# Performance work log

Hardware: AMD Instinct MI355X
Metric: run time of the kernel (lower is better)

The kernel has to match this reference:

```python
import jax, jax.numpy as jnp
import numpy as np

B, S, R, H = 64, 256, 196, 1024

def setup_inputs() -> dict:
    key = jax.random.key(0)
    ks = jax.random.split(key, 12)
    s = 0.02
    return {
        "dns_feature": jax.random.normal(ks[0], (B, S, H), jnp.float32),
        "img_features": jax.random.normal(ks[1], (B, R, H), jnp.float32),
        "W_dns1": jax.random.normal(ks[2], (H, H), jnp.float32) * s,
        "b_dns1": jax.random.normal(ks[3], (H,), jnp.float32) * s,
        "W_img1": jax.random.normal(ks[4], (H, H), jnp.float32) * s,
        "w_att1": jax.random.normal(ks[5], (2 * H,), jnp.float32) * s,
        "b_att1": jax.random.normal(ks[6], (), jnp.float32) * s,
        "W_dns2": jax.random.normal(ks[7], (H, H), jnp.float32) * s,
        "W_img2": jax.random.normal(ks[8], (H, H), jnp.float32) * s,
        "b_img2": jax.random.normal(ks[9], (H,), jnp.float32) * s,
        "w_att2": jax.random.normal(ks[10], (2 * H,), jnp.float32) * s,
        "b_att2": jax.random.normal(ks[11], (), jnp.float32) * s,
    }

def reference(dns_feature, img_features, W_dns1, b_dns1, W_img1, w_att1, b_att1,
              W_dns2, W_img2, b_img2, w_att2, b_att2):
    h = W_dns1.shape[0]
    # --- stage 1: textual attention (img queries over dns positions) ---
    # tanh(concat([img_proj, dns_proj])) then 2H->1 linear decomposes into
    # per-side dot products + broadcast add (repeat is position-wise redundant).
    dns_p1 = jnp.tanh(jnp.einsum('bsh,oh->bso', dns_feature, W_dns1) + b_dns1)  # (B,S,H)
    img_p1 = jnp.tanh(jnp.einsum('brh,oh->bro', img_features, W_img1))          # (B,R,H)
    s_img = img_p1 @ w_att1[:h]   # (B,R)  concat order: [img, dns]
    s_dns = dns_p1 @ w_att1[h:]   # (B,S)
    scores1 = s_img[:, :, None] + s_dns[:, None, :] + b_att1                    # (B,R,S)
    a1 = jax.nn.softmax(scores1, axis=-1)
    att_dns = jnp.einsum('brs,bsh->brh', a1, dns_feature)                       # (B,R,H)
    # --- stage 2: visual attention (attended-dns queries over img regions) ---
    dns_p2 = jnp.tanh(jnp.einsum('brh,oh->bro', att_dns, W_dns2))               # (B,R,H)
    img_p2 = jnp.tanh(jnp.einsum('brh,oh->bro', img_features, W_img2) + b_img2) # (B,R,H)
    t_dns = dns_p2 @ w_att2[:h]   # (B,R)  concat order: [dns, img]
    t_img = img_p2 @ w_att2[h:]   # (B,R)
    scores2 = t_dns[:, :, None] + t_img[:, None, :] + b_att2                    # (B,R,R)
    a2 = jax.nn.softmax(scores2, axis=-1)
    att_img = jnp.einsum('bij,bjh->bih', a2, img_features)                      # (B,R,H)
    return att_img, att_dns
```

## Files before the change

kernel.cpp:

```cpp
#include <hip/hip_runtime.h>

#define Hdim 1024
#define BB 64
#define SS 256
#define RR 196
#define MD (BB * SS)
#define MI (BB * RR)

typedef __attribute__((ext_vector_type(8))) short short8;
typedef __attribute__((ext_vector_type(4))) float floatx4;
typedef unsigned short us;

__device__ __forceinline__ unsigned short f2bf(float f) {
  unsigned int u = __float_as_uint(f);
  unsigned int r = 0x7FFFu + ((u >> 16) & 1u);
  return (unsigned short)((u + r) >> 16);
}

__device__ __forceinline__ float fast_tanh(float x) {
  x = fminf(15.f, fmaxf(-15.f, x));
  float e = __expf(2.f * x);
  return (e - 1.f) / (e + 1.f);
}

#define GLOAD16(g, l) __builtin_amdgcn_global_load_lds( \
    (const __attribute__((address_space(1))) unsigned int*)(g), \
    (__attribute__((address_space(3))) unsigned int*)(l), 16, 0, 0)

#define MEMFENCE asm volatile("" ::: "memory")

__global__ __launch_bounds__(256) void prep_kernel(
    const float4* __restrict__ dns, const float4* __restrict__ img,
    const float4* __restrict__ Wd1, const float4* __restrict__ Wi2,
    uint4* __restrict__ dns_bf, uint4* __restrict__ img_bf,
    uint4* __restrict__ wd1_bf, uint4* __restrict__ wi2_bf,
    float4* __restrict__ scz)
{
  constexpr int N0 = (MD * Hdim) / 8;
  constexpr int N1 = N0 + (MI * Hdim) / 8;
  constexpr int N2 = N1 + (Hdim * Hdim) / 8;
  constexpr int N3 = N2 + (Hdim * Hdim) / 8;
  constexpr int N4 = N3 + (MD + MI) / 8;
  const int stride = gridDim.x * 256;
  for (int i = blockIdx.x * 256 + threadIdx.x; i < N4; i += stride) {
    if (i < N3) {
      const float4* src; uint4* dst; int li;
      if (i < N0)      { src = dns; dst = dns_bf; li = i; }
      else if (i < N1) { src = img; dst = img_bf; li = i - N0; }
      else if (i < N2) { src = Wd1; dst = wd1_bf; li = i - N1; }
      else             { src = Wi2; dst = wi2_bf; li = i - N2; }
      const float4 a = src[2 * li];
      const float4 b = src[2 * li + 1];
      uint4 o;
      o.x = (unsigned)f2bf(a.x) | ((unsigned)f2bf(a.y) << 16);
      o.y = (unsigned)f2bf(a.z) | ((unsigned)f2bf(a.w) << 16);
      o.z = (unsigned)f2bf(b.x) | ((unsigned)f2bf(b.y) << 16);
      o.w = (unsigned)f2bf(b.z) | ((unsigned)f2bf(b.w) << 16);
      dst[li] = o;
    } else {
      const int li = i - N3;
      const float4 z4 = {0.f, 0.f, 0.f, 0.f};
      scz[2 * li]     = z4;
      scz[2 * li + 1] = z4;
    }
  }
}

#define NB1 ((MD / 256) * 4)
#define NB2 ((MI / 256) * 4)

__global__ __launch_bounds__(512, 2) void gemm_score_8p(
    const us* __restrict__ X1, const us* __restrict__ W1,
    const float* __restrict__ bias1, const float* __restrict__ v1, float* sc1,
    const us* __restrict__ X2, const us* __restrict__ W2,
    const float* __restrict__ bias2, const float* __restrict__ v2, float* sc2)
{
  __shared__ us LDS[65536];

  const int nwg = gridDim.x;
  const int q = nwg >> 3, rr = nwg & 7;
  const int xcd = blockIdx.x & 7, idx = blockIdx.x >> 3;
  const int wg = (xcd < rr ? xcd * (q + 1) : rr * (q + 1) + (xcd - rr) * q) + idx;

  const us* Xb; const us* Wb; const float* bias; const float* vatt; float* scores;
  int mt, nt;
  if (wg < NB1) {
    Xb = X1; Wb = W1; bias = bias1; vatt = v1; scores = sc1;
    mt = wg >> 2; nt = wg & 3;
  } else {
    const int w2 = wg - NB1;
    Xb = X2; Wb = W2; bias = bias2; vatt = v2; scores = sc2;
    mt = w2 >> 2; nt = w2 & 3;
  }
  const long m0 = (long)mt * 256;
  const long n0 = (long)nt * 256;

  const int tid  = threadIdx.x;
  const int lane = tid & 63;
  const int w    = tid >> 6;
  const int wm   = w >> 2;
  const int wn   = w & 3;

  const int srow = lane >> 3;
  const int scol = ((lane & 7) ^ srow) * 8;
  const us* gA = Xb + (m0 + w * 8 + srow) * Hdim + scol;
  const us* gB = Wb + (n0 + w * 8 + srow) * Hdim + scol;
  const int ldl = (w * 64 + lane) * 8;

#define STAGE_A(d, h, kk) do { \
    GLOAD16(gA + ((h) * 128 + 0) * Hdim + (kk),  &LDS[(d) * 16384 + (h) * 8192 + 0    + ldl]); \
    GLOAD16(gA + ((h) * 128 + 64) * Hdim + (kk), &LDS[(d) * 16384 + (h) * 8192 + 4096 + ldl]); } while (0)
#define STAGE_B(d, h, kk) do { \
    GLOAD16(gB + ((h) * 128 + 0) * Hdim + (kk),  &LDS[32768 + (d) * 16384 + (h) * 8192 + 0    + ldl]); \
    GLOAD16(gB + ((h) * 128 + 64) * Hdim + (kk), &LDS[32768 + (d) * 16384 + (h) * 8192 + 4096 + ldl]); } while (0)

  floatx4 acc[8][4];
  #pragma unroll
  for (int i = 0; i < 8; ++i)
    #pragma unroll
    for (int j = 0; j < 4; ++j)
      acc[i][j] = (floatx4){0.f, 0.f, 0.f, 0.f};

  const int frow = lane & 15;
  const int g    = lane >> 4;
  const int sw   = frow & 7;
  const int aRow = wm * 8192 + frow * 64;
  const int bRow = (wn >> 1) * 8192 + ((wn & 1) * 64 + frow) * 64;

  STAGE_A(0, 0, 0); STAGE_A(0, 1, 0); STAGE_B(0, 0, 0); STAGE_B(0, 1, 0);
  asm volatile("s_waitcnt vmcnt(0)" ::: "memory");
  MEMFENCE; __builtin_amdgcn_s_barrier(); MEMFENCE;

  #pragma unroll 1
  for (int T = 0; T < 16; ++T) {
    const int d   = T & 1;
    const int kk1 = (T + 1) * 64;
    const int Ab  = d * 16384 + aRow;
    const int Bb  = 32768 + d * 16384 + bRow;
    const int s0  = (g ^ sw) * 8;
    const int s1  = ((4 + g) ^ sw) * 8;
    short8 a[4], b0[4], b1[4];

    if (T < 15) { STAGE_A(d ^ 1, 0, kk1); STAGE_A(d ^ 1, 1, kk1); }
    #pragma unroll
    for (int mf = 0; mf < 4; ++mf) a[mf] = *(const short8*)&LDS[Ab + mf * 1024 + s0];
    #pragma unroll
    for (int nf = 0; nf < 4; ++nf) b0[nf] = *(const short8*)&LDS[Bb + nf * 1024 + s0];
    __builtin_amdgcn_s_setprio(1);
    #pragma unroll
    for (int mf = 0; mf < 4; ++mf)
      #pragma unroll
      for (int nf = 0; nf < 4; ++nf)
        acc[mf][nf] = __builtin_amdgcn_mfma_f32_16x16x32_bf16(a[mf], b0[nf], acc[mf][nf], 0, 0, 0);
    __builtin_amdgcn_s_setprio(0);
    MEMFENCE; __builtin_amdgcn_s_barrier(); MEMFENCE;

    if (T < 15) { STAGE_B(d ^ 1, 0, kk1); STAGE_B(d ^ 1, 1, kk1); }
    #pragma unroll
    for (int mf = 0; mf < 4; ++mf) a[mf] = *(const short8*)&LDS[Ab + (mf + 4) * 1024 + s0];
    __builtin_amdgcn_s_setprio(1);
    #pragma unroll
    for (int mf = 0; mf < 4; ++mf)
      #pragma unroll
      for (int nf = 0; nf < 4; ++nf)
        acc[mf + 4][nf] = __builtin_amdgcn_mfma_f32_16x16x32_bf16(a[mf], b0[nf], acc[mf + 4][nf], 0, 0, 0);
    __builtin_amdgcn_s_setprio(0);
    MEMFENCE; __builtin_amdgcn_s_barrier(); MEMFENCE;

    #pragma unroll
    for (int mf = 0; mf < 4; ++mf) a[mf] = *(const short8*)&LDS[Ab + mf * 1024 + s1];
    #pragma unroll
    for (int nf = 0; nf < 4; ++nf) b1[nf] = *(const short8*)&LDS[Bb + nf * 1024 + s1];
    __builtin_amdgcn_s_setprio(1);
    #pragma unroll
    for (int mf = 0; mf < 4; ++mf)
      #pragma unroll
      for (int nf = 0; nf < 4; ++nf)
        acc[mf][nf] = __builtin_amdgcn_mfma_f32_16x16x32_bf16(a[mf], b1[nf], acc[mf][nf], 0, 0, 0);
    __builtin_amdgcn_s_setprio(0);
    MEMFENCE; __builtin_amdgcn_s_barrier(); MEMFENCE;

    #pragma unroll
    for (int mf = 0; mf < 4; ++mf) a[mf] = *(const short8*)&LDS[Ab + (mf + 4) * 1024 + s1];
    __builtin_amdgcn_s_setprio(1);
    #pragma unroll
    for (int mf = 0; mf < 4; ++mf)
      #pragma unroll
      for (int nf = 0; nf < 4; ++nf)
        acc[mf + 4][nf] = __builtin_amdgcn_mfma_f32_16x16x32_bf16(a[mf], b1[nf], acc[mf + 4][nf], 0, 0, 0);
    __builtin_amdgcn_s_setprio(0);
    asm volatile("s_waitcnt vmcnt(0)" ::: "memory");
    MEMFENCE; __builtin_amdgcn_s_barrier(); MEMFENCE;
  }

  const int rgrp = lane >> 4;
  #pragma unroll
  for (int mf = 0; mf < 8; ++mf) {
    float part[4] = {0.f, 0.f, 0.f, 0.f};
    #pragma unroll
    for (int nf = 0; nf < 4; ++nf) {
      const int n = (int)n0 + wn * 64 + nf * 16 + (lane & 15);
      const float bi = bias[n];
      const float vv = vatt[n];
      #pragma unroll
      for (int j = 0; j < 4; ++j)
        part[j] += fast_tanh(acc[mf][nf][j] + bi) * vv;
    }
    #pragma unroll
    for (int j = 0; j < 4; ++j) {
      float s = part[j];
      s += __shfl_xor(s, 1);
      s += __shfl_xor(s, 2);
      s += __shfl_xor(s, 4);
      s += __shfl_xor(s, 8);
      if ((lane & 15) == 0) {
        const int m = (int)m0 + wm * 128 + mf * 16 + rgrp * 4 + j;
        atomicAdd(&scores[m], s);
      }
    }
  }
#undef STAGE_A
#undef STAGE_B
}

__global__ __launch_bounds__(256) void attend_bcast(
    const float* __restrict__ sc_d, const us* __restrict__ dns_bf,
    const float* __restrict__ sc_i, const us* __restrict__ img_bf,
    float* __restrict__ out)
{
  __shared__ float p[256];
  __shared__ float red[256];
  const int b  = blockIdx.x;
  const int h0 = blockIdx.y * 512;
  const int z  = blockIdx.z;
  const int L  = z ? RR : SS;
  const float* scores = z ? sc_i : sc_d;
  const us*    feat   = z ? img_bf : dns_bf;
  float* outp = out + (z ? (size_t)0 : (size_t)BB * RR * Hdim);
  const int t = threadIdx.x;

  const float sc = (t < L) ? scores[b * L + t] : -1e30f;
  red[t] = sc;
  __syncthreads();
  for (int off = 128; off > 0; off >>= 1) {
    if (t < off) red[t] = fmaxf(red[t], red[t + off]);
    __syncthreads();
  }
  const float mx = red[0];
  __syncthreads();
  const float e = (t < L) ? __expf(sc - mx) : 0.f;
  red[t] = e;
  __syncthreads();
  for (int off = 128; off > 0; off >>= 1) {
    if (t < off) red[t] += red[t + off];
    __syncthreads();
  }
  p[t] = e / red[0];
  __syncthreads();

  const int h = h0 + 2 * t;
  const us* fb = feat + (size_t)b * L * Hdim + h;
  float a0 = 0.f, a1 = 0.f;
  #pragma unroll 8
  for (int s = 0; s < L; ++s) {
    const unsigned u = *(const unsigned*)(fb + (size_t)s * Hdim);
    const float f0 = __uint_as_float(u << 16);
    const float f1 = __uint_as_float(u & 0xffff0000u);
    a0 += p[s] * f0;
    a1 += p[s] * f1;
  }

  float* ob = outp + (size_t)b * RR * Hdim + h;
  const float2 v = make_float2(a0, a1);
  #pragma unroll 4
  for (int r = 0; r < RR; ++r)
    *(float2*)(ob + (size_t)r * Hdim) = v;
}

__global__ __launch_bounds__(256) void gemm_score(
    const float* __restrict__ X, const float* __restrict__ W,
    const float* __restrict__ bias, const float* __restrict__ vatt,
    float* __restrict__ scores)
{
  __shared__ us Ash[128 * 32];
  __shared__ us Bsh[128 * 32];
  const int tid  = threadIdx.x;
  const int lane = tid & 63;
  const int wave = tid >> 6;
  const int waveM = (wave >> 1) * 64;
  const int waveN = (wave & 1) * 64;
  const long m0 = (long)blockIdx.x * 128;
  const long n0 = (long)blockIdx.y * 128;
  const int ldRow   = tid >> 3;
  const int ldChunk = (tid & 7) * 4;

  floatx4 acc[4][4];
  #pragma unroll
  for (int i = 0; i < 4; ++i)
    #pragma unroll
    for (int j = 0; j < 4; ++j)
      acc[i][j] = (floatx4){0.f, 0.f, 0.f, 0.f};

  const int frow = lane & 15;
  const int fk   = (lane >> 4) * 8;

  for (int k0 = 0; k0 < Hdim; k0 += 32) {
    __syncthreads();
    #pragma unroll
    for (int p = 0; p < 4; ++p) {
      const int r = ldRow + p * 32;
      const float4 av = *(const float4*)&X[(m0 + r) * Hdim + k0 + ldChunk];
      const float4 bv = *(const float4*)&W[(n0 + r) * Hdim + k0 + ldChunk];
      uint2 ap, bp;
      ap.x = (unsigned)f2bf(av.x) | ((unsigned)f2bf(av.y) << 16);
      ap.y = (unsigned)f2bf(av.z) | ((unsigned)f2bf(av.w) << 16);
      bp.x = (unsigned)f2bf(bv.x) | ((unsigned)f2bf(bv.y) << 16);
      bp.y = (unsigned)f2bf(bv.z) | ((unsigned)f2bf(bv.w) << 16);
      *(uint2*)&Ash[r * 32 + ldChunk] = ap;
      *(uint2*)&Bsh[r * 32 + ldChunk] = bp;
    }
    __syncthreads();
    short8 afr[4], bfr[4];
    #pragma unroll
    for (int mf = 0; mf < 4; ++mf)
      afr[mf] = *(const short8*)&Ash[(waveM + mf * 16 + frow) * 32 + fk];
    #pragma unroll
    for (int nf = 0; nf < 4; ++nf)
      bfr[nf] = *(const short8*)&Bsh[(waveN + nf * 16 + frow) * 32 + fk];
    #pragma unroll
    for (int mf = 0; mf < 4; ++mf)
      #pragma unroll
      for (int nf = 0; nf < 4; ++nf)
        acc[mf][nf] = __builtin_amdgcn_mfma_f32_16x16x32_bf16(afr[mf], bfr[nf], acc[mf][nf], 0, 0, 0);
  }

  const int rgrp = lane >> 4;
  #pragma unroll
  for (int mf = 0; mf < 4; ++mf) {
    float part[4] = {0.f, 0.f, 0.f, 0.f};
    #pragma unroll
    for (int nf = 0; nf < 4; ++nf) {
      const int n = (int)n0 + waveN + nf * 16 + (lane & 15);
      const float bi = bias[n];
      const float vv = vatt[n];
      #pragma unroll
      for (int j = 0; j < 4; ++j)
        part[j] += fast_tanh(acc[mf][nf][j] + bi) * vv;
    }
    #pragma unroll
    for (int j = 0; j < 4; ++j) {
      float s = part[j];
      s += __shfl_xor(s, 1);
      s += __shfl_xor(s, 2);
      s += __shfl_xor(s, 4);
      s += __shfl_xor(s, 8);
      if ((lane & 15) == 0) {
        const int m = (int)m0 + waveM + mf * 16 + rgrp * 4 + j;
        atomicAdd(&scores[m], s);
      }
    }
  }
}

template <int L>
__global__ __launch_bounds__(256) void softmax_attend(
    const float* __restrict__ scores, const float* __restrict__ feat,
    float* __restrict__ attended)
{
  __shared__ float p[256];
  __shared__ float red[256];
  const int b  = blockIdx.x;
  const int h0 = blockIdx.y * 256;
  const int t  = threadIdx.x;

  const float sc = (t < L) ? scores[b * L + t] : -1e30f;
  red[t] = sc;
  __syncthreads();
  for (int off = 128; off > 0; off >>= 1) {
    if (t < off) red[t] = fmaxf(red[t], red[t + off]);
    __syncthreads();
  }
  const float mx = red[0];
  __syncthreads();
  const float e = (t < L) ? __expf(sc - mx) : 0.f;
  red[t] = e;
  __syncthreads();
  for (int off = 128; off > 0; off >>= 1) {
    if (t < off) red[t] += red[t + off];
    __syncthreads();
  }
  p[t] = e / red[0];
  __syncthreads();

  const int h = h0 + t;
  const float* fb = feat + (size_t)b * L * Hdim + h;
  float acc = 0.f;
  #pragma unroll 4
  for (int s = 0; s < L; ++s)
    acc += p[s] * fb[(size_t)s * Hdim];
  attended[b * Hdim + h] = acc;
}

__global__ __launch_bounds__(256) void broadcast_out(
    const float4* __restrict__ att_img, const float4* __restrict__ att_dns,
    float4* __restrict__ out)
{
  const int H4 = Hdim / 4;
  const long region_sz = (long)BB * RR * H4;
  const long total = 2 * region_sz;
  for (long i = (long)blockIdx.x * blockDim.x + threadIdx.x; i < total;
       i += (long)gridDim.x * blockDim.x) {
    const int region = (i >= region_sz);
    const long rem = i - (long)region * region_sz;
    const int b  = (int)(rem / (RR * H4));
    const int h4 = (int)(rem % H4);
    const float4* src = region ? att_dns : att_img;
    out[i] = src[b * H4 + h4];
  }
}

extern "C" void kernel_launch(void* const* d_in, const int* in_sizes, int n_in,
                              void* d_out, int out_size, void* d_ws, size_t ws_size,
                              hipStream_t stream) {
  const float* dns    = (const float*)d_in[0];
  const float* img    = (const float*)d_in[1];
  const float* W_dns1 = (const float*)d_in[2];
  const float* b_dns1 = (const float*)d_in[3];
  const float* w_att1 = (const float*)d_in[5];
  const float* W_img2 = (const float*)d_in[8];
  const float* b_img2 = (const float*)d_in[9];
  const float* w_att2 = (const float*)d_in[10];

  const size_t dnsB = (size_t)MD * Hdim * 2;
  const size_t imgB = (size_t)MI * Hdim * 2;
  const size_t wB   = (size_t)Hdim * Hdim * 2;
  const size_t scoresB = (16384 + 12544) * sizeof(float);
  const size_t need = dnsB + imgB + 2 * wB + scoresB;

  dim3 blk(256);

  if (ws_size >= need) {
    char* cur = (char*)d_ws;
    us* dns_bf = (us*)cur; cur += dnsB;
    us* img_bf = (us*)cur; cur += imgB;
    us* Wd1_bf = (us*)cur; cur += wB;
    us* Wi2_bf = (us*)cur; cur += wB;
    float* s_dns = (float*)cur;
    float* t_img = s_dns + 16384;

    prep_kernel<<<2048, blk, 0, stream>>>(
        (const float4*)dns, (const float4*)img,
        (const float4*)W_dns1, (const float4*)W_img2,
        (uint4*)dns_bf, (uint4*)img_bf, (uint4*)Wd1_bf, (uint4*)Wi2_bf,
        (float4*)s_dns);

    gemm_score_8p<<<dim3(NB1 + NB2), dim3(512), 0, stream>>>(
        dns_bf, Wd1_bf, b_dns1, w_att1 + Hdim, s_dns,
        img_bf, Wi2_bf, b_img2, w_att2 + Hdim, t_img);

    attend_bcast<<<dim3(BB, Hdim / 512, 2), blk, 0, stream>>>(
        s_dns, dns_bf, t_img, img_bf, (float*)d_out);
  } else {
    float* ws    = (float*)d_ws;
    float* s_dns = ws;
    float* t_img = ws + 16384;
    float* att_d = ws + 16384 + 12544;
    float* att_i = att_d + BB * Hdim;

    hipMemsetAsync(s_dns, 0, (16384 + 12544) * sizeof(float), stream);

    gemm_score<<<dim3(MD / 128, Hdim / 128), blk, 0, stream>>>(
        dns, W_dns1, b_dns1, w_att1 + Hdim, s_dns);
    gemm_score<<<dim3(MI / 128, Hdim / 128), blk, 0, stream>>>(
        img, W_img2, b_img2, w_att2 + Hdim, t_img);

    softmax_attend<SS><<<dim3(BB, Hdim / 256), blk, 0, stream>>>(s_dns, dns, att_d);
    softmax_attend<RR><<<dim3(BB, Hdim / 256), blk, 0, stream>>>(t_img, img, att_i);

    broadcast_out<<<2048, blk, 0, stream>>>((const float4*)att_i, (const float4*)att_d,
                                            (float4*)d_out);
  }
}
```

Before: 154.6 us.

## Halve GEMM K-tile to 32 to cut LDS and raise occupancy

Reduces the K-step of the fused projection/score GEMM from 64 to 32, halving the LDS footprint, and retunes the global-to-LDS staging and swizzle for 32-wide rows. Launch bounds request more resident blocks per CU so that more workgroups can overlap. The cost is twice as many loop iterations with more barriers per unit of work, and tighter register limits that may cause spilling of the large accumulator array.

```diff
diff --git a/kernel.cpp b/kernel.cpp
--- a/kernel.cpp
+++ b/kernel.cpp
@@ -69,13 +69,13 @@
 #define NB1 ((MD / 256) * 4)
 #define NB2 ((MI / 256) * 4)
 
-__global__ __launch_bounds__(512, 2) void gemm_score_8p(
+__global__ __launch_bounds__(512, 4) void gemm_score_8p(
     const us* __restrict__ X1, const us* __restrict__ W1,
     const float* __restrict__ bias1, const float* __restrict__ v1, float* sc1,
     const us* __restrict__ X2, const us* __restrict__ W2,
     const float* __restrict__ bias2, const float* __restrict__ v2, float* sc2)
 {
-  __shared__ us LDS[65536];
+  __shared__ us LDS[32768];
 
   const int nwg = gridDim.x;
   const int q = nwg >> 3, rr = nwg & 7;
@@ -101,18 +101,20 @@
   const int wm   = w >> 2;
   const int wn   = w & 3;
 
-  const int srow = lane >> 3;
-  const int scol = ((lane & 7) ^ srow) * 8;
-  const us* gA = Xb + (m0 + w * 8 + srow) * Hdim + scol;
-  const us* gB = Wb + (n0 + w * 8 + srow) * Hdim + scol;
-  const int ldl = (w * 64 + lane) * 8;
-
-#define STAGE_A(d, h, kk) do { \
-    GLOAD16(gA + ((h) * 128 + 0) * Hdim + (kk),  &LDS[(d) * 16384 + (h) * 8192 + 0    + ldl]); \
-    GLOAD16(gA + ((h) * 128 + 64) * Hdim + (kk), &LDS[(d) * 16384 + (h) * 8192 + 4096 + ldl]); } while (0)
-#define STAGE_B(d, h, kk) do { \
-    GLOAD16(gB + ((h) * 128 + 0) * Hdim + (kk),  &LDS[32768 + (d) * 16384 + (h) * 8192 + 0    + ldl]); \
-    GLOAD16(gB + ((h) * 128 + 64) * Hdim + (kk), &LDS[32768 + (d) * 16384 + (h) * 8192 + 4096 + ldl]); } while (0)
+  const int srow4 = (lane >> 2) & 3;
+  const int scol  = ((lane & 3) ^ srow4) * 8;
+  const int tid8  = tid * 8;
+  const us* gA0 = Xb + (m0 + 0   + (tid >> 2)) * Hdim + scol;
+  const us* gA1 = Xb + (m0 + 128 + (tid >> 2)) * Hdim + scol;
+  const us* gB0 = Wb + (n0 + 0   + (tid >> 2)) * Hdim + scol;
+  const us* gB1 = Wb + (n0 + 128 + (tid >> 2)) * Hdim + scol;
+
+#define STAGE_A(d, kk) do { \
+    GLOAD16(gA0 + (kk), &LDS[(d) * 8192 + 0    + tid8]); \
+    GLOAD16(gA1 + (kk), &LDS[(d) * 8192 + 4096 + tid8]); } while (0)
+#define STAGE_B(d, kk) do { \
+    GLOAD16(gB0 + (kk), &LDS[16384 + (d) * 8192 + 0    + tid8]); \
+    GLOAD16(gB1 + (kk), &LDS[16384 + (d) * 8192 + 4096 + tid8]); } while (0)
 
   floatx4 acc[8][4];
   #pragma unroll
@@ -123,71 +125,46 @@
 
   const int frow = lane & 15;
   const int g    = lane >> 4;
-  const int sw   = frow & 7;
-  const int aRow = wm * 8192 + frow * 64;
-  const int bRow = (wn >> 1) * 8192 + ((wn & 1) * 64 + frow) * 64;
-
-  STAGE_A(0, 0, 0); STAGE_A(0, 1, 0); STAGE_B(0, 0, 0); STAGE_B(0, 1, 0);
+  const int slotE = ((g ^ (frow & 3)) * 8);
+  const int aRow = (wm * 128 + frow) * 32 + slotE;
+  const int bRow = 16384 + (wn * 64 + frow) * 32 + slotE;
+
+  STAGE_A(0, 0); STAGE_B(0, 0);
   asm volatile("s_waitcnt vmcnt(0)" ::: "memory");
   MEMFENCE; __builtin_amdgcn_s_barrier(); MEMFENCE;
 
   #pragma unroll 1
-  for (int T = 0; T < 16; ++T) {
+  for (int T = 0; T < 32; ++T) {
     const int d   = T & 1;
-    const int kk1 = (T + 1) * 64;
-    const int Ab  = d * 16384 + aRow;
-    const int Bb  = 32768 + d * 16384 + bRow;
-    const int s0  = (g ^ sw) * 8;
-    const int s1  = ((4 + g) ^ sw) * 8;
-    short8 a[4], b0[4], b1[4];
-
-    if (T < 15) { STAGE_A(d ^ 1, 0, kk1); STAGE_A(d ^ 1, 1, kk1); }
-    #pragma unroll
-    for (int mf = 0; mf < 4; ++mf) a[mf] = *(const short8*)&LDS[Ab + mf * 1024 + s0];
-    #pragma unroll
-    for (int nf = 0; nf < 4; ++nf) b0[nf] = *(const short8*)&LDS[Bb + nf * 1024 + s0];
+    const int kk1 = (T + 1) * 32;
+    const int Ab  = d * 8192 + aRow;
+    const int Bb  = d * 8192 + bRow;
+    short8 a[4], b[4];
+
+    #pragma unroll
+    for (int mf = 0; mf < 4; ++mf) a[mf] = *(const short8*)&LDS[Ab + mf * 512];
+    #pragma unroll
+    for (int nf = 0; nf < 4; ++nf) b[nf] = *(const short8*)&LDS[Bb + nf * 512];
+    if (T < 31) { STAGE_A(d ^ 1, kk1); STAGE_B(d ^ 1, kk1); }
+    MEMFENCE; __builtin_amdgcn_s_barrier(); MEMFENCE;
     __builtin_amdgcn_s_setprio(1);
     #pragma unroll
     for (int mf = 0; mf < 4; ++mf)
       #pragma unroll
       for (int nf = 0; nf < 4; ++nf)
-        acc[mf][nf] = __builtin_amdgcn_mfma_f32_16x16x32_bf16(a[mf], b0[nf], acc[mf][nf], 0, 0, 0);
+        acc[mf][nf] = __builtin_amdgcn_mfma_f32_16x16x32_bf16(a[mf], b[nf], acc[mf][nf], 0, 0, 0);
     __builtin_amdgcn_s_setprio(0);
     MEMFENCE; __builtin_amdgcn_s_barrier(); MEMFENCE;
 
-    if (T < 15) { STAGE_B(d ^ 1, 0, kk1); STAGE_B(d ^ 1, 1, kk1); }
-    #pragma unroll
-    for (int mf = 0; mf < 4; ++mf) a[mf] = *(const short8*)&LDS[Ab + (mf + 4) * 1024 + s0];
+    #pragma unroll
+    for (int mf = 0; mf < 4; ++mf) a[mf] = *(const short8*)&LDS[Ab + (mf + 4) * 512];
+    MEMFENCE; __builtin_amdgcn_s_barrier(); MEMFENCE;
     __builtin_amdgcn_s_setprio(1);
     #pragma unroll
     for (int mf = 0; mf < 4; ++mf)
       #pragma unroll
       for (int nf = 0; nf < 4; ++nf)
-        acc[mf + 4][nf] = __builtin_amdgcn_mfma_f32_16x16x32_bf16(a[mf], b0[nf], acc[mf + 4][nf], 0, 0, 0);
-    __builtin_amdgcn_s_setprio(0);
-    MEMFENCE; __builtin_amdgcn_s_barrier(); MEMFENCE;
-
-    #pragma unroll
-    for (int mf = 0; mf < 4; ++mf) a[mf] = *(const short8*)&LDS[Ab + mf * 1024 + s1];
-    #pragma unroll
-    for (int nf = 0; nf < 4; ++nf) b1[nf] = *(const short8*)&LDS[Bb + nf * 1024 + s1];
-    __builtin_amdgcn_s_setprio(1);
-    #pragma unroll
-    for (int mf = 0; mf < 4; ++mf)
-      #pragma unroll
-      for (int nf = 0; nf < 4; ++nf)
-        acc[mf][nf] = __builtin_amdgcn_mfma_f32_16x16x32_bf16(a[mf], b1[nf], acc[mf][nf], 0, 0, 0);
-    __builtin_amdgcn_s_setprio(0);
-    MEMFENCE; __builtin_amdgcn_s_barrier(); MEMFENCE;
-
-    #pragma unroll
-    for (int mf = 0; mf < 4; ++mf) a[mf] = *(const short8*)&LDS[Ab + (mf + 4) * 1024 + s1];
-    __builtin_amdgcn_s_setprio(1);
-    #pragma unroll
-    for (int mf = 0; mf < 4; ++mf)
-      #pragma unroll
-      for (int nf = 0; nf < 4; ++nf)
-        acc[mf + 4][nf] = __builtin_amdgcn_mfma_f32_16x16x32_bf16(a[mf], b1[nf], acc[mf + 4][nf], 0, 0, 0);
+        acc[mf + 4][nf] = __builtin_amdgcn_mfma_f32_16x16x32_bf16(a[mf], b[nf], acc[mf + 4][nf], 0, 0, 0);
     __builtin_amdgcn_s_setprio(0);
     asm volatile("s_waitcnt vmcnt(0)" ::: "memory");
     MEMFENCE; __builtin_amdgcn_s_barrier(); MEMFENCE;
```

Measured after the change: 497.7 us. +222.0%, slower.
